# Kernel tuning notes

Hardware: AMD Instinct MI355X
Metric: run time of the kernel (lower is better)

The kernel has to match this reference:

```python
import jax, jax.numpy as jnp
import numpy as np

N = 10000; E = 320000; B = 262144
F_NODE = 64; F_EDGE = 8; H = 4; C = 32
EVO_IN = C * 4 * H + 1      # 513
EVO_HID = 256; EVO_DIM = 64
FLOW_IN = EVO_DIM + 5       # 69
FLOW_HID = 256
SLOPE = 0.01                # torch LeakyReLU default slope
GAT_SLOPE = 0.2             # GATv2 attention LeakyReLU slope
EPS = 1e-5                  # BatchNorm eps


def setup_inputs() -> dict:
    key = jax.random.key(0)
    ks = iter(jax.random.split(key, 64))
    def nrm(shape, scale=1.0):
        return jax.random.normal(next(ks), shape, jnp.float32) * scale
    inp = {}
    inp['x1'] = nrm((N, F_NODE))
    inp['edge_index1'] = jax.random.randint(next(ks), (2, E), 0, N)
    inp['edge_attr1'] = nrm((E, F_EDGE))
    inp['x2'] = nrm((N, F_NODE))
    inp['edge_index2'] = jax.random.randint(next(ks), (2, E), 0, N)
    inp['edge_attr2'] = nrm((E, F_EDGE))
    inp['dist_m'] = jax.random.uniform(next(ks), (N, N), jnp.float32)
    inp['node_visit'] = jax.random.uniform(next(ks), (N, 2), jnp.float32)
    inp['od_nodes'] = jax.random.randint(next(ks), (B, 2), 0, N)
    # GATv2Conv params per snapshot: lin_l, lin_r (bias=True), lin_edge (bias=False), att [H,C], out bias [H*C]
    for p in ('g1', 'g2'):
        s = 1.0 / np.sqrt(F_NODE)
        inp[p + '_Wl'] = nrm((H * C, F_NODE), s)
        inp[p + '_bl'] = jnp.zeros((H * C,), jnp.float32)
        inp[p + '_Wr'] = nrm((H * C, F_NODE), s)
        inp[p + '_br'] = jnp.zeros((H * C,), jnp.float32)
        inp[p + '_We'] = nrm((H * C, F_EDGE), 1.0 / np.sqrt(F_EDGE))
        inp[p + '_att'] = nrm((H, C), 1.0 / np.sqrt(C))
        inp[p + '_bias'] = jnp.zeros((H * C,), jnp.float32)
    # EvoEmbedding (all Linear bias=False)
    inp['e_W1'] = nrm((EVO_HID, EVO_IN), 1.0 / np.sqrt(EVO_IN))
    inp['e_W2'] = nrm((EVO_HID, EVO_HID), 1.0 / np.sqrt(EVO_HID))
    inp['e_W3'] = nrm((EVO_HID, EVO_HID), 1.0 / np.sqrt(EVO_HID))
    inp['e_W4'] = nrm((EVO_HID // 2, EVO_HID), 1.0 / np.sqrt(EVO_HID))
    inp['e_Wout'] = nrm((EVO_DIM, EVO_HID // 2), 1.0 / np.sqrt(EVO_HID // 2))
    # FlowGenerator (Linear bias=False) + BatchNorm affine params
    inp['f_W1'] = nrm((FLOW_HID, FLOW_IN), 1.0 / np.sqrt(FLOW_IN))
    inp['f_W2'] = nrm((FLOW_HID, FLOW_HID), 1.0 / np.sqrt(FLOW_HID))
    inp['f_W3'] = nrm((FLOW_HID, FLOW_HID), 1.0 / np.sqrt(FLOW_HID))
    inp['f_W4'] = nrm((FLOW_HID // 2, FLOW_HID), 1.0 / np.sqrt(FLOW_HID))
    inp['f_Wout'] = nrm((1, FLOW_HID // 2), 1.0 / np.sqrt(FLOW_HID // 2))
    inp['f_g1'] = jnp.ones((FLOW_HID,), jnp.float32);  inp['f_b1'] = jnp.zeros((FLOW_HID,), jnp.float32)
    inp['f_g2'] = jnp.ones((FLOW_HID,), jnp.float32);  inp['f_b2'] = jnp.zeros((FLOW_HID,), jnp.float32)
    inp['f_g3'] = jnp.ones((FLOW_HID,), jnp.float32);  inp['f_b3'] = jnp.zeros((FLOW_HID,), jnp.float32)
    inp['f_g4'] = jnp.ones((FLOW_HID // 2,), jnp.float32); inp['f_b4'] = jnp.zeros((FLOW_HID // 2,), jnp.float32)
    return inp


def _gatv2(x, ei, ea, Wl, bl, Wr, br, We, att, bias):
    src, dst = ei[0], ei[1]
    # self-loops with fill_value='mean': per-target mean of incoming edge_attr
    deg = jax.ops.segment_sum(jnp.ones_like(dst, jnp.float32), dst, N)
    mean_attr = jax.ops.segment_sum(ea, dst, N) / jnp.maximum(deg, 1.0)[:, None]
    loops = jnp.arange(N)
    s = jnp.concatenate([src, loops]); d = jnp.concatenate([dst, loops])
    eaf = jnp.concatenate([ea, mean_attr], axis=0)            # [E+N, F_EDGE]
    xl = (x @ Wl.T + bl).reshape(N, H, C)                     # source transform
    xr = (x @ Wr.T + br).reshape(N, H, C)                     # target transform
    em = (eaf @ We.T).reshape(-1, H, C)
    msg = jax.nn.leaky_relu(xl[s] + xr[d] + em, GAT_SLOPE)    # [E+N, H, C]
    scr = jnp.einsum('ehc,hc->eh', msg, att)                  # [E+N, H]
    mx = jax.ops.segment_max(scr, d, N)
    ex = jnp.exp(scr - mx[d])
    den = jax.ops.segment_sum(ex, d, N)
    alpha = ex / den[d]                                       # softmax over incoming edges
    out = jax.ops.segment_sum(alpha[:, :, None] * xl[s], d, N).reshape(N, H * C) + bias
    return jax.nn.relu(out), alpha


def _evo(v, W1, W2, W3, W4, Wout):
    h = jax.nn.leaky_relu(v @ W1.T, SLOPE)
    h = jax.nn.leaky_relu(h @ W2.T, SLOPE)
    h = jax.nn.leaky_relu(h @ W3.T, SLOPE)
    h = jax.nn.leaky_relu(h @ W4.T, SLOPE)
    return h @ Wout.T


def _bn(x, g, b):
    mu = x.mean(0)
    var = x.var(0)
    return (x - mu) * jax.lax.rsqrt(var + EPS) * g + b


def _flow(v, W1, W2, W3, W4, Wout, g1, b1, g2, b2, g3, b3, g4, b4):
    h = jax.nn.leaky_relu(_bn(v @ W1.T, g1, b1), SLOPE)
    h = jax.nn.leaky_relu(_bn(h @ W2.T, g2, b2), SLOPE)
    h = jax.nn.leaky_relu(_bn(h @ W3.T, g3, b3), SLOPE)
    h = jax.nn.leaky_relu(_bn(h @ W4.T, g4, b4), SLOPE)
    return (h @ Wout.T).squeeze(-1)


def reference(x1, edge_index1, edge_attr1, x2, edge_index2, edge_attr2, dist_m, node_visit, od_nodes,
              g1_Wl, g1_bl, g1_Wr, g1_br, g1_We, g1_att, g1_bias,
              g2_Wl, g2_bl, g2_Wr, g2_br, g2_We, g2_att, g2_bias,
              e_W1, e_W2, e_W3, e_W4, e_Wout,
              f_W1, f_W2, f_W3, f_W4, f_Wout,
              f_g1, f_b1, f_g2, f_b2, f_g3, f_b3, f_g4, f_b4):
    n1, a1 = _gatv2(x1, edge_index1, edge_attr1, g1_Wl, g1_bl, g1_Wr, g1_br, g1_We, g1_att, g1_bias)
    n2, a2 = _gatv2(x2, edge_index2, edge_attr2, g2_Wl, g2_bl, g2_Wr, g2_br, g2_We, g2_att, g2_bias)
    o = od_nodes[:, 0]; dn = od_nodes[:, 1]
    dist = dist_m[o, dn][:, None]                              # fused gather replacing python loop
    feat = jnp.concatenate([n1[o], n1[dn], n2[o], n2[dn], dist], axis=1)  # [B, 513]
    evo = _evo(feat, e_W1, e_W2, e_W3, e_W4, e_Wout)           # [B, EVO_DIM]
    # NOTE: original uses node_visit[:,0] for BOTH o_visit and d_visit (kept faithful)
    ov = node_visit[o, 0:1]; dv = node_visit[dn, 0:1]
    ovn = node_visit[o, 1:2]; dvn = node_visit[dn, 1:2]
    cat = jnp.concatenate([evo, ov, dv, ovn, dvn, dist], axis=1)  # [B, 69]
    inferred = _flow(cat, f_W1, f_W2, f_W3, f_W4, f_Wout, f_g1, f_b1, f_g2, f_b2, f_g3, f_b3, f_g4, f_b4)
    return (inferred, a1, a2, evo)
```

## Files before the change

kernel.cpp:

```cpp
#include <hip/hip_runtime.h>

typedef unsigned short u16;
typedef unsigned int u32;

#define NN 10000
#define NE 320000
#define ET 330000
#define NB 262144

typedef __attribute__((ext_vector_type(8))) short bf16x8;
typedef __attribute__((ext_vector_type(4))) float f32x4;

__device__ __forceinline__ u16 f2b(float f) {
  u32 u = __float_as_uint(f);
  u += 0x7fffu + ((u >> 16) & 1u);
  return (u16)(u >> 16);
}
__device__ __forceinline__ float b2f(u16 h) {
  return __uint_as_float(((u32)h) << 16);
}
__device__ __forceinline__ float lrelu(float v, float s) { return v > 0.f ? v : v * s; }

__device__ __forceinline__ void g2lds16(const void* g, void* l) {
  __builtin_amdgcn_global_load_lds((const __attribute__((address_space(1))) void*)g,
                                   (__attribute__((address_space(3))) void*)l, 16, 0, 0);
}

template <int N> __device__ __forceinline__ void waitv() {
  if constexpr (N == 0) asm volatile("s_waitcnt vmcnt(0)" ::: "memory");
  else if constexpr (N == 1) asm volatile("s_waitcnt vmcnt(1)" ::: "memory");
  else if constexpr (N == 2) asm volatile("s_waitcnt vmcnt(2)" ::: "memory");
  else if constexpr (N == 3) asm volatile("s_waitcnt vmcnt(3)" ::: "memory");
  else if constexpr (N == 4) asm volatile("s_waitcnt vmcnt(4)" ::: "memory");
  else if constexpr (N == 5) asm volatile("s_waitcnt vmcnt(5)" ::: "memory");
  else asm volatile("s_waitcnt vmcnt(6)" ::: "memory");
}
__device__ __forceinline__ void waitl0() { asm volatile("s_waitcnt lgkmcnt(0)" ::: "memory"); }
__device__ __forceinline__ void fence() { asm volatile("" ::: "memory"); }

__global__ __launch_bounds__(256) void k_prep(const float* __restrict__ eW2, const float* __restrict__ eW3,
                                              const float* __restrict__ eW4, const float* __restrict__ eWo,
                                              const float* __restrict__ fW1, const float* __restrict__ fW2,
                                              const float* __restrict__ fW3, const float* __restrict__ fW4,
                                              const float* __restrict__ eW1,
                                              u16* eW2b, u16* eW3b, u16* eW4b, u16* eWob,
                                              u16* fW2b, u16* fW3b, u16* fW4b,
                                              float* W1T, float* w512, u16* combW) {
  const int blk = blockIdx.x, tid = threadIdx.x;
  if (blk < 256) {
    int t = blk * 256 + tid; eW2b[t] = f2b(eW2[t]);
  } else if (blk < 512) {
    int t = (blk - 256) * 256 + tid; eW3b[t] = f2b(eW3[t]);
  } else if (blk < 640) {
    int t = (blk - 512) * 256 + tid; eW4b[t] = f2b(eW4[t]);
  } else if (blk < 672) {
    int t = (blk - 640) * 256 + tid; eWob[t] = f2b(eWo[t]);
  } else if (blk < 928) {
    int t = (blk - 672) * 256 + tid; fW2b[t] = f2b(fW2[t]);
  } else if (blk < 1184) {
    int t = (blk - 928) * 256 + tid; fW3b[t] = f2b(fW3[t]);
  } else if (blk < 1312) {
    int t = (blk - 1184) * 256 + tid; fW4b[t] = f2b(fW4[t]);
  } else if (blk < 1568) {
    int m = blk - 1312;
    for (int k = tid; k < 512; k += 256) W1T[(size_t)k * 256 + m] = eW1[(size_t)m * 513 + k];
  } else if (blk == 1568) {
    w512[tid] = eW1[(size_t)tid * 513 + 512];
  } else {
    int m = blk - 1569;
    int k = tid;
    if (k < 160) {
      float v = 0.f;
      if (k < 128) {
        const float* fr = fW1 + (size_t)m * 69;
        for (int j = 0; j < 64; ++j) v += fr[j] * eWo[(size_t)j * 128 + k];
      } else if (k < 133) {
        v = fW1[(size_t)m * 69 + 64 + (k - 128)];
      }
      combW[(size_t)m * 160 + k] = f2b(v);
    }
  }
}

__global__ __launch_bounds__(256) void k_sprep(const int* __restrict__ od, const float* __restrict__ dm,
                                               const float* __restrict__ nv,
                                               float* __restrict__ distb, u16* __restrict__ bufC) {
  int b = blockIdx.x * 256 + threadIdx.x;
  int o = od[b * 2], d = od[b * 2 + 1];
  float dist = dm[(size_t)o * NN + d];
  distb[b] = dist;
  u16 tmp[32];
  tmp[0] = f2b(nv[o * 2]);
  tmp[1] = f2b(nv[d * 2]);
  tmp[2] = f2b(nv[o * 2 + 1]);
  tmp[3] = f2b(nv[d * 2 + 1]);
  tmp[4] = f2b(dist);
#pragma unroll
  for (int k = 5; k < 32; ++k) tmp[k] = 0;
  u16* p = bufC + (size_t)b * 160 + 128;
#pragma unroll
  for (int k = 0; k < 4; ++k) *(bf16x8*)(p + k * 8) = *(bf16x8*)(tmp + k * 8);
}

__global__ __launch_bounds__(256) void k_count(const int* __restrict__ ei, int* __restrict__ cnt) {
  int t = blockIdx.x * 256 + threadIdx.x;
  if (t >= ET) return;
  int d = (t < NE) ? ei[NE + t] : (t - NE);
  atomicAdd(&cnt[d], 1);
}

__global__ __launch_bounds__(1024) void k_scan(const int* __restrict__ cnt, int* __restrict__ cs) {
  __shared__ int part[1024];
  int tid = threadIdx.x;
  int base = tid * 10;
  int local[10];
  int s = 0;
#pragma unroll
  for (int i = 0; i < 10; ++i) {
    int idx = base + i;
    int v = (idx < NN) ? cnt[idx] : 0;
    local[i] = s; s += v;
  }
  part[tid] = s;
  __syncthreads();
  for (int off = 1; off < 1024; off <<= 1) {
    int v = (tid >= off) ? part[tid - off] : 0;
    __syncthreads();
    part[tid] += v;
    __syncthreads();
  }
  int pre = (tid > 0) ? part[tid - 1] : 0;
#pragma unroll
  for (int i = 0; i < 10; ++i) {
    int idx = base + i;
    if (idx < NN) cs[idx] = pre + local[i];
  }
  if (tid == 1023) cs[NN] = part[1023];
}

__global__ __launch_bounds__(256) void k_fill(const int* __restrict__ ei, const int* __restrict__ cs,
                                              int* __restrict__ wr, int2* __restrict__ csr) {
  int t = blockIdx.x * 256 + threadIdx.x;
  if (t >= ET) return;
  int s, d;
  if (t < NE) { s = ei[t]; d = ei[NE + t]; } else { s = t - NE; d = s; }
  int pos = atomicAdd(&wr[d], 1);
  csr[cs[d] + pos] = make_int2(t, s);
}

__global__ __launch_bounds__(256) void k_asum(const int2* __restrict__ csr, const int* __restrict__ cs,
                                              const float* __restrict__ ea, float* __restrict__ asum) {
  int wid = (blockIdx.x * 256 + threadIdx.x) >> 6;
  int lane = threadIdx.x & 63;
  int beg = cs[wid], end = cs[wid + 1];
  int j = lane & 7, slot = lane >> 3;
  float acc = 0.f;
  for (int i = beg + slot; i < end; i += 8) {
    int e = csr[i].x;
    if (e < NE) acc += ea[(size_t)e * 8 + j];
  }
  acc += __shfl_xor(acc, 8);
  acc += __shfl_xor(acc, 16);
  acc += __shfl_xor(acc, 32);
  if (lane < 8) {
    float dr = (float)(end - beg - 1);
    asum[(size_t)wid * 8 + lane] = acc / fmaxf(dr, 1.f);
  }
}

__global__ __launch_bounds__(256) void k_xlr(const float* __restrict__ x,
                                             const float* __restrict__ Wl, const float* __restrict__ bl,
                                             const float* __restrict__ Wr, const float* __restrict__ br,
                                             float* __restrict__ xl, float* __restrict__ xr) {
  __shared__ float sx[128];
  int nb = blockIdx.x * 2;
  for (int i = threadIdx.x; i < 128; i += 256) sx[i] = x[(size_t)nb * 64 + i];
  __syncthreads();
  int half = threadIdx.x >> 7;
  int node = nb + half;
  int m = threadIdx.x & 127;
  const float* xv = sx + (half << 6);
  float al = bl[m], ar = br[m];
  const float* wl = Wl + (size_t)m * 64;
  const float* wr = Wr + (size_t)m * 64;
#pragma unroll 8
  for (int k = 0; k < 64; ++k) { float xk = xv[k]; al += xk * wl[k]; ar += xk * wr[k]; }
  xl[(size_t)node * 128 + m] = al;
  xr[(size_t)node * 128 + m] = ar;
}

__global__ __launch_bounds__(256) void k_scr(const float* __restrict__ xl, const float* __restrict__ xr,
                                             const int* __restrict__ ei, const float* __restrict__ ea,
                                             const float* __restrict__ mattr,
                                             const float* __restrict__ We, const float* __restrict__ att,
                                             float* __restrict__ scr) {
  const int lane = threadIdx.x & 63;
  const int sub = lane & 31;
  const int half = lane >> 5;
  float4 w0[4], w1[4];
#pragma unroll
  for (int c = 0; c < 4; ++c) {
    const float* wp = We + (size_t)(sub * 4 + c) * 8;
    w0[c] = *(const float4*)wp;
    w1[c] = *(const float4*)(wp + 4);
  }
  const float4 attv = *(const float4*)(att + sub * 4);
  const int gw = (blockIdx.x * 256 + threadIdx.x) >> 6;
  const int nw = gridDim.x * 4;
  for (int p = gw; p < ET / 2; p += nw) {
    int e = p * 2 + half;
    int s, d; const float* ap;
    if (e < NE) { s = ei[e]; d = ei[NE + e]; ap = ea + (size_t)e * 8; }
    else { s = e - NE; d = s; ap = mattr + (size_t)(e - NE) * 8; }
    float4 a0 = *(const float4*)ap;
    float4 a1 = *(const float4*)(ap + 4);
    float4 xlv = *(const float4*)(xl + (size_t)s * 128 + sub * 4);
    float4 xrv = *(const float4*)(xr + (size_t)d * 128 + sub * 4);
    const float* xle = (const float*)&xlv;
    const float* xre = (const float*)&xrv;
    const float* ate = (const float*)&attv;
    float psum = 0.f;
#pragma unroll
    for (int c = 0; c < 4; ++c) {
      float em = a0.x * w0[c].x + a0.y * w0[c].y + a0.z * w0[c].z + a0.w * w0[c].w
               + a1.x * w1[c].x + a1.y * w1[c].y + a1.z * w1[c].z + a1.w * w1[c].w;
      float v = xle[c] + xre[c] + em;
      v = v > 0.f ? v : 0.2f * v;
      psum += v * ate[c];
    }
    psum += __shfl_xor(psum, 1);
    psum += __shfl_xor(psum, 2);
    psum += __shfl_xor(psum, 4);
    if ((sub & 7) == 0) scr[(size_t)e * 4 + (sub >> 3)] = psum;
  }
}

__global__ __launch_bounds__(256) void k_nodered(const float* __restrict__ scr, const int2* __restrict__ csr,
                                                 const int* __restrict__ cs, const float* __restrict__ xl,
                                                 const float* __restrict__ bias,
                                                 float* __restrict__ m_out, float* __restrict__ den_out,
                                                 float* __restrict__ nout) {
  int d = (blockIdx.x * 256 + threadIdx.x) >> 6;
  int lane = threadIdx.x & 63;
  int h0 = lane >> 5;
  int beg = cs[d], end = cs[d + 1];
  float mx0 = -3.4e38f, mx1 = -3.4e38f;
  for (int i = beg; i < end; ++i) {
    int e = csr[i].x;
    mx0 = fmaxf(mx0, scr[(size_t)e * 4 + h0]);
    mx1 = fmaxf(mx1, scr[(size_t)e * 4 + h0 + 2]);
  }
  float acc0 = 0.f, acc1 = 0.f, dn0 = 0.f, dn1 = 0.f;
  for (int i = beg; i < end; ++i) {
    int2 es = csr[i];
    float ex0 = __expf(scr[(size_t)es.x * 4 + h0] - mx0);
    float ex1 = __expf(scr[(size_t)es.x * 4 + h0 + 2] - mx1);
    dn0 += ex0; dn1 += ex1;
    const float* xp = xl + (size_t)es.y * 128;
    acc0 += ex0 * xp[lane];
    acc1 += ex1 * xp[64 + lane];
  }
  if (lane == 0 || lane == 32) {
    m_out[d * 4 + h0] = mx0;     m_out[d * 4 + h0 + 2] = mx1;
    den_out[d * 4 + h0] = dn0;   den_out[d * 4 + h0 + 2] = dn1;
  }
  nout[(size_t)d * 128 + lane] = fmaxf(acc0 / dn0 + bias[lane], 0.f);
  nout[(size_t)d * 128 + 64 + lane] = fmaxf(acc1 / dn1 + bias[64 + lane], 0.f);
}

__global__ __launch_bounds__(256) void k_alpha(const float* __restrict__ scr, const int* __restrict__ ei,
                                               const float* __restrict__ m, const float* __restrict__ den,
                                               float* __restrict__ aout) {
  int t = blockIdx.x * 256 + threadIdx.x;
  if (t >= ET * 4) return;
  int e = t >> 2, h = t & 3;
  int d = (e < NE) ? ei[NE + e] : (e - NE);
  aout[t] = __expf(scr[t] - m[d * 4 + h]) / den[d * 4 + h];
}

__global__ __launch_bounds__(256) void k_qtab(const float* __restrict__ n1, const float* __restrict__ n2,
                                              const float* __restrict__ W1T,
                                              u16* __restrict__ Qo, u16* __restrict__ Qd) {
  __shared__ float s1[2048], s2[2048];
  int nb = blockIdx.x * 16;
  for (int i = threadIdx.x; i < 2048; i += 256) {
    s1[i] = n1[(size_t)nb * 128 + i];
    s2[i] = n2[(size_t)nb * 128 + i];
  }
  __syncthreads();
  int m = threadIdx.x;
  float qo[16], qd[16];
#pragma unroll
  for (int i = 0; i < 16; ++i) { qo[i] = 0.f; qd[i] = 0.f; }
#pragma unroll 2
  for (int k = 0; k < 128; ++k) {
    float w0 = W1T[(size_t)k * 256 + m];
    float w1 = W1T[(size_t)(128 + k) * 256 + m];
    float w2 = W1T[(size_t)(256 + k) * 256 + m];
    float w3 = W1T[(size_t)(384 + k) * 256 + m];
#pragma unroll
    for (int i = 0; i < 16; ++i) {
      float a = s1[i * 128 + k], b = s2[i * 128 + k];
      qo[i] += a * w0 + b * w2;
      qd[i] += a * w1 + b * w3;
    }
  }
#pragma unroll
  for (int i = 0; i < 16; ++i) {
    Qo[(size_t)(nb + i) * 256 + m] = f2b(qo[i]);
    Qd[(size_t)(nb + i) * 256 + m] = f2b(qd[i]);
  }
}

template <int NF, int EPI, int BNA>
__global__ __launch_bounds__(512) void gemm256(const u16* __restrict__ A, const u16* __restrict__ W,
                                               int K, size_t lda,
                                               u16* __restrict__ obf, int ld_bf,
                                               float* __restrict__ stats,
                                               const float* __restrict__ stin, const float* __restrict__ gg,
                                               const float* __restrict__ bb, float invB) {
  constexpr int M = NF * 64;
  constexpr int CPW = 2 + NF / 2;
  __shared__ alignas(16) u16 Alds[2][256 * 32];
  __shared__ alignas(16) u16 Blds[2][M * 32];
  __shared__ float sS[256], sT[256];
  const int tid = threadIdx.x;
  const int lane = tid & 63;
  const int w = tid >> 6;
  const int wr = w >> 2, wc = w & 3;
  const size_t rowBase = (size_t)blockIdx.x * 256;

  if (BNA) {
    for (int c = tid; c < K; c += 512) {
      float mu = stin[c] * invB;
      float var = stin[K + c] * invB - mu * mu;
      float sc = rsqrtf(var + 1e-5f) * gg[c];
      sS[c] = sc;
      sT[c] = bb[c] - mu * sc;
    }
    __syncthreads();
  }

  f32x4 acc[8][NF];
  const f32x4 z4 = {0.f, 0.f, 0.f, 0.f};
#pragma unroll
  for (int m = 0; m < 8; ++m)
#pragma unroll
    for (int n = 0; n < NF; ++n) acc[m][n] = z4;

  const int crow = lane >> 2;
  const int ccol = (lane & 3) << 3;
  const int KT = K >> 5;

  auto stage = [&](int buf, int kb) {
#pragma unroll
    for (int i = 0; i < CPW; ++i) {
      const int c = w * CPW + i;
      if (c < 16) {
        const u16* src = A + (rowBase + (c << 4) + crow) * lda + kb + ccol;
        g2lds16(src, &Alds[buf][(c << 4) << 5]);
// ... 137 lines not shown
  };
  auto writeA = [&](int buf, int kb, bf16x8 r0, bf16x8 r1, bf16x8 r2, bf16x8 r3) {
    float dist = sDist[arow];
    bf16x8 w0, w1;
#pragma unroll
    for (int j = 0; j < 8; ++j) {
      float v = b2f((u16)r0[j]) + b2f((u16)r2[j]) + dist * sW[kb + acol + j];
      w0[j] = (short)f2b(lrelu(v, 0.01f));
      float v2 = b2f((u16)r1[j]) + b2f((u16)r3[j]) + dist * sW[kb + acol + 8 + j];
      w1[j] = (short)f2b(lrelu(v2, 0.01f));
    }
    *(bf16x8*)&Alds[buf][arow * 32 + acol] = w0;
    *(bf16x8*)&Alds[buf][arow * 32 + acol + 8] = w1;
  };

  f32x4 acc[8][4];
  const f32x4 z4 = {0.f, 0.f, 0.f, 0.f};
#pragma unroll
  for (int m = 0; m < 8; ++m)
#pragma unroll
    for (int n = 0; n < 4; ++n) acc[m][n] = z4;

  bf16x8 p0, p1, p2, p3;
  {
    bf16x8 c0, c1, c2, c3;
    loadA(0, c0, c1, c2, c3);
    writeA(0, 0, c0, c1, c2, c3);
  }
  stageB(0, 0);
  fence();
  loadA(32, p0, p1, p2, p3);
  fence();
  waitv<4>();
  waitl0();
  __builtin_amdgcn_s_barrier();

  int cur = 0;
  for (int kt = 0; kt < KT; ++kt) {
    const int kb = kt << 5;
    const bool hasN = kt + 1 < KT, hasNN = kt + 2 < KT;
    bf16x8 bfr[4];
#pragma unroll
    for (int n = 0; n < 4; ++n)
      bfr[n] = *(const bf16x8*)&Blds[cur][((((wc << 2) + n) << 4) + lr) * 32 + lk];
    if (hasN) stageB(cur ^ 1, kb + 32);
    fence();
    bf16x8 q0, q1, q2, q3;
    if (hasNN) loadA(kb + 64, q0, q1, q2, q3);
    fence();
#pragma unroll
    for (int m = 0; m < 8; ++m) {
      bf16x8 af = *(const bf16x8*)&Alds[cur][(((wr << 7) + (m << 4) + lr) << 5) + lk];
#pragma unroll
      for (int n = 0; n < 4; ++n)
        acc[m][n] = __builtin_amdgcn_mfma_f32_16x16x32_bf16(af, bfr[n], acc[m][n], 0, 0, 0);
    }
    if (hasN) {
      if (hasNN) waitv<6>(); else waitv<2>();
      writeA(cur ^ 1, kb + 32, p0, p1, p2, p3);
      p0 = q0; p1 = q1; p2 = q2; p3 = q3;
      if (hasNN) waitv<4>(); else waitv<0>();
      waitl0();
    }
    __builtin_amdgcn_s_barrier();
    cur ^= 1;
  }

#pragma unroll
  for (int m = 0; m < 8; ++m) {
#pragma unroll
    for (int n = 0; n < 4; ++n) {
      const int col = (wc << 6) + (n << 4) + lr;
#pragma unroll
      for (int j = 0; j < 4; ++j) {
        const size_t row = rowBase + (wr << 7) + (m << 4) + (lg << 2) + j;
        float v = acc[m][n][j];
        v = v > 0.f ? v : v * 0.01f;
        obf[row * 256 + col] = f2b(v);
      }
    }
  }
}

template <int NF>
__global__ __launch_bounds__(256) void gemm_f32out(const u16* __restrict__ A, const u16* __restrict__ W,
                                                   int K, size_t lda, int M, float* __restrict__ of32) {
  constexpr int CW = NF * 16;
  __shared__ alignas(16) u16 Alds[2][128 * 32];
  __shared__ alignas(16) u16 Blds[2][CW * 2 * 32];
  const int lane = threadIdx.x & 63;
  const int w = threadIdx.x >> 6;
  const int wr = w >> 1, wc = w & 1;
  const size_t rowBase = (size_t)blockIdx.x * 128;

  f32x4 acc[4][NF];
  const f32x4 z4 = {0.f, 0.f, 0.f, 0.f};
#pragma unroll
  for (int m = 0; m < 4; ++m)
#pragma unroll
    for (int n = 0; n < NF; ++n) acc[m][n] = z4;

  const int sr = (w << 4) + (lane >> 2);
  const int sc = (lane & 3) << 3;
  const int KT = K >> 5;

  auto stage = [&](int buf, int kb) {
#pragma unroll
    for (int i = 0; i < 2; ++i) {
      const u16* src = A + (rowBase + (i << 6) + sr) * lda + kb + sc;
      g2lds16(src, &Alds[buf][((i << 6) + (w << 4)) << 5]);
    }
#pragma unroll
    for (int i = 0; i < NF / 2; ++i) {
      const u16* src = W + (size_t)((i << 6) + sr) * K + kb + sc;
      g2lds16(src, &Blds[buf][((i << 6) + (w << 4)) << 5]);
    }
  };

  stage(0, 0);
  int cur = 0;
  for (int kt = 0; kt < KT; ++kt) {
    if (kt + 1 < KT) {
      stage(cur ^ 1, (kt + 1) << 5);
      asm volatile("s_waitcnt vmcnt(3)" ::: "memory");
    } else {
      asm volatile("s_waitcnt vmcnt(0)" ::: "memory");
    }
    __builtin_amdgcn_s_barrier();
    const int lr = lane & 15, lk = (lane >> 4) << 3;
    bf16x8 af[4], bfr[NF];
#pragma unroll
    for (int m = 0; m < 4; ++m)
      af[m] = *(const bf16x8*)&Alds[cur][(((wr << 6) + (m << 4) + lr) << 5) + lk];
#pragma unroll
    for (int n = 0; n < NF; ++n)
      bfr[n] = *(const bf16x8*)&Blds[cur][((wc * CW + (n << 4) + lr) << 5) + lk];
#pragma unroll
    for (int m = 0; m < 4; ++m)
#pragma unroll
      for (int n = 0; n < NF; ++n)
        acc[m][n] = __builtin_amdgcn_mfma_f32_16x16x32_bf16(af[m], bfr[n], acc[m][n], 0, 0, 0);
    __builtin_amdgcn_s_barrier();
    cur ^= 1;
  }

  const int lr = lane & 15, lg = lane >> 4;
#pragma unroll
  for (int m = 0; m < 4; ++m) {
#pragma unroll
    for (int n = 0; n < NF; ++n) {
      const int col = wc * CW + (n << 4) + lr;
      if (col >= M) continue;
#pragma unroll
      for (int j = 0; j < 4; ++j) {
        const size_t row = rowBase + (wr << 6) + (m << 4) + (lg << 2) + j;
        of32[row * M + col] = acc[m][n][j];
      }
    }
  }
}

__global__ __launch_bounds__(256) void k_fout4(const u16* __restrict__ pre, const float* __restrict__ st,
                                               const float* __restrict__ g, const float* __restrict__ b,
                                               const float* __restrict__ W, float* __restrict__ out,
                                               float invB) {
  __shared__ float smu[128], srs[128], sg[128], sb[128], sw[128];
  if (threadIdx.x < 128) {
    int c = threadIdx.x;
    float mu = st[c] * invB;
    float var = st[128 + c] * invB - mu * mu;
    smu[c] = mu;
    srs[c] = rsqrtf(var + 1e-5f);
    sg[c] = g[c];
    sb[c] = b[c];
    sw[c] = W[c];
  }
  __syncthreads();
  int bi = blockIdx.x * 256 + threadIdx.x;
  const u16* hp = pre + (size_t)bi * 128;
  float acc = 0.f;
#pragma unroll
  for (int k = 0; k < 128; k += 8) {
    bf16x8 u = *(const bf16x8*)(hp + k);
#pragma unroll
    for (int j = 0; j < 8; ++j) {
      int c = k + j;
      float v = (b2f((u16)u[j]) - smu[c]) * srs[c] * sg[c] + sb[c];
      v = b2f(f2b(lrelu(v, 0.01f)));
      acc += v * sw[c];
    }
  }
  out[bi] = acc;
}

extern "C" void kernel_launch(void* const* d_in, const int* in_sizes, int n_in,
                              void* d_out, int out_size, void* d_ws, size_t ws_size,
                              hipStream_t stream) {
  (void)in_sizes; (void)n_in; (void)out_size; (void)ws_size;

  const float* x[2] = {(const float*)d_in[0], (const float*)d_in[3]};
  const int* ei[2] = {(const int*)d_in[1], (const int*)d_in[4]};
  const float* ea[2] = {(const float*)d_in[2], (const float*)d_in[5]};
  const float* dm = (const float*)d_in[6];
  const float* nv = (const float*)d_in[7];
  const int* od = (const int*)d_in[8];
  const float* Wl[2] = {(const float*)d_in[9], (const float*)d_in[16]};
  const float* bl[2] = {(const float*)d_in[10], (const float*)d_in[17]};
  const float* Wr[2] = {(const float*)d_in[11], (const float*)d_in[18]};
  const float* br[2] = {(const float*)d_in[12], (const float*)d_in[19]};
  const float* We[2] = {(const float*)d_in[13], (const float*)d_in[20]};
  const float* att[2] = {(const float*)d_in[14], (const float*)d_in[21]};
  const float* bia[2] = {(const float*)d_in[15], (const float*)d_in[22]};
  const float* eW1 = (const float*)d_in[23];
  const float* eW2 = (const float*)d_in[24];
  const float* eW3 = (const float*)d_in[25];
  const float* eW4 = (const float*)d_in[26];
  const float* eWo = (const float*)d_in[27];
  const float* fW1 = (const float*)d_in[28];
  const float* fW2 = (const float*)d_in[29];
  const float* fW3 = (const float*)d_in[30];
  const float* fW4 = (const float*)d_in[31];
  const float* fWo = (const float*)d_in[32];
  const float* fg[4] = {(const float*)d_in[33], (const float*)d_in[35], (const float*)d_in[37], (const float*)d_in[39]};
  const float* fb[4] = {(const float*)d_in[34], (const float*)d_in[36], (const float*)d_in[38], (const float*)d_in[40]};

  float* out_inf = (float*)d_out;
  float* out_a1 = out_inf + NB;
  float* out_a2 = out_a1 + (size_t)ET * 4;
  float* out_evo = out_a2 + (size_t)ET * 4;

  char* base = (char*)d_ws;
  size_t cur = 0;
  auto carve = [&](size_t bytes) -> char* {
    char* p = base + cur;
    cur += (bytes + 255) & ~(size_t)255;
    return p;
  };
  u16* bufA = (u16*)carve((size_t)NB * 256 * 2);
  u16* bufB = (u16*)carve((size_t)NB * 256 * 2);
  u16* bufC = (u16*)carve((size_t)NB * 160 * 2);
  float* n1 = (float*)carve((size_t)NN * 128 * 4);
  float* n2 = (float*)carve((size_t)NN * 128 * 4);
  u16* Qob = (u16*)carve((size_t)NN * 256 * 2);
  u16* Qdb = (u16*)carve((size_t)NN * 256 * 2);
  float* xl = (float*)carve((size_t)NN * 128 * 4);
  float* xr = (float*)carve((size_t)NN * 128 * 4);
  int* cnt = (int*)carve((size_t)(NN + 1) * 4);
  int* wr = (int*)carve((size_t)NN * 4);
  int* cs = (int*)carve((size_t)(NN + 1) * 4);
  int2* csr = (int2*)carve((size_t)ET * 8);
  float* m_out = (float*)carve((size_t)NN * 4 * 4);
  float* den_out = (float*)carve((size_t)NN * 4 * 4);
  float* asum = (float*)carve((size_t)NN * 8 * 4);
  float* scr = (float*)carve((size_t)ET * 4 * 4);
  float* distb = (float*)carve((size_t)NB * 4);
  float* w512 = (float*)carve(1024);
  float* W1T = (float*)carve(512 * 256 * 4);
  float* stats = (float*)carve(1792 * 4);
  float* st[4] = {stats, stats + 512, stats + 1024, stats + 1536};
  u16* eW2b = (u16*)carve(256 * 256 * 2);
  u16* eW3b = (u16*)carve(256 * 256 * 2);
  u16* eW4b = (u16*)carve(128 * 256 * 2);
  u16* eWob = (u16*)carve(64 * 128 * 2);
  u16* fW2b = (u16*)carve(256 * 256 * 2);
  u16* fW3b = (u16*)carve(256 * 256 * 2);
  u16* fW4b = (u16*)carve(128 * 256 * 2);
  u16* combW = (u16*)carve(256 * 160 * 2);

  k_prep<<<1825, 256, 0, stream>>>(eW2, eW3, eW4, eWo, fW1, fW2, fW3, fW4, eW1,
                                   eW2b, eW3b, eW4b, eWob, fW2b, fW3b, fW4b,
                                   W1T, w512, combW);
  hipMemsetAsync(stats, 0, 1792 * 4, stream);
  k_sprep<<<NB / 256, 256, 0, stream>>>(od, dm, nv, distb, bufC);

  float* nout[2] = {n1, n2};
  float* aout[2] = {out_a1, out_a2};
  const int EB = (ET + 255) / 256;
  const size_t cwSpan = (size_t)((char*)wr - (char*)cnt) + (size_t)NN * 4;
  for (int gi = 0; gi < 2; ++gi) {
    hipMemsetAsync(cnt, 0, cwSpan, stream);
    k_count<<<EB, 256, 0, stream>>>(ei[gi], cnt);
    k_scan<<<1, 1024, 0, stream>>>(cnt, cs);
    k_fill<<<EB, 256, 0, stream>>>(ei[gi], cs, wr, csr);
    k_asum<<<NN / 4, 256, 0, stream>>>(csr, cs, ea[gi], asum);
    k_xlr<<<NN / 2, 256, 0, stream>>>(x[gi], Wl[gi], bl[gi], Wr[gi], br[gi], xl, xr);
    k_scr<<<2048, 256, 0, stream>>>(xl, xr, ei[gi], ea[gi], asum, We[gi], att[gi], scr);
    k_nodered<<<NN / 4, 256, 0, stream>>>(scr, csr, cs, xl, bia[gi], m_out, den_out, nout[gi]);
    k_alpha<<<(ET * 4 + 255) / 256, 256, 0, stream>>>(scr, ei[gi], m_out, den_out, aout[gi]);
  }

  k_qtab<<<NN / 16, 256, 0, stream>>>(n1, n2, W1T, Qob, Qdb);

  const float invB = 1.0f / (float)NB;
  const int GB = NB / 256;
  gemm256_evo<<<GB, 512, 0, stream>>>(eW2b, bufA, Qob, Qdb, od, distb, w512);
  gemm256<4, 0, 0><<<GB, 512, 0, stream>>>(bufA, eW3b, 256, 256, bufB, 256, nullptr,
                                           nullptr, nullptr, nullptr, 0.f);
  gemm256<2, 0, 0><<<GB, 512, 0, stream>>>(bufB, eW4b, 256, 256, bufC, 160, nullptr,
                                           nullptr, nullptr, nullptr, 0.f);
  gemm_f32out<2><<<NB / 128, 256, 0, stream>>>(bufC, eWob, 128, 160, 64, out_evo);

  gemm256<4, 1, 0><<<GB, 512, 0, stream>>>(bufC, combW, 160, 160, bufA, 256, st[0],
                                           nullptr, nullptr, nullptr, 0.f);
  gemm256<4, 1, 1><<<GB, 512, 0, stream>>>(bufA, fW2b, 256, 256, bufB, 256, st[1],
                                           st[0], fg[0], fb[0], invB);
  gemm256<4, 1, 1><<<GB, 512, 0, stream>>>(bufB, fW3b, 256, 256, bufA, 256, st[2],
                                           st[1], fg[1], fb[1], invB);
  gemm256<2, 1, 1><<<GB, 512, 0, stream>>>(bufA, fW4b, 256, 256, bufB, 128, st[3],
                                           st[2], fg[2], fb[2], invB);
  k_fout4<<<NB / 256, 256, 0, stream>>>(bufB, st[3], fg[3], fb[3], fWo, out_inf, invB);
}
```

Measured before the change: 1.386 ms.

## Batch both GAT snapshots into single launches and fuse evo-out with flow layer-1 GEMM

Each graph-preprocessing and GATv2 kernel now handles both snapshots in one launch, with a doubled grid and per-graph buffers, instead of a two-iteration host loop. This halves the launch count and gives small kernels more parallelism. The evo output projection and the first flow layer share the same input (bufC), so they are merged into one 320-column GEMM. That GEMM writes fp32 evo output for the first 64 columns and bf16 pre-activations plus BatchNorm stats for the remaining 256. The cost is more workspace memory and a larger per-block accumulator tile, which may lower occupancy.

Measured after the change: 1.316 ms. -5.0%, faster.

```diff
diff --git a/kernel.cpp b/kernel.cpp
--- a/kernel.cpp
+++ b/kernel.cpp
@@ -43,9 +43,9 @@
                                               const float* __restrict__ fW1, const float* __restrict__ fW2,
                                               const float* __restrict__ fW3, const float* __restrict__ fW4,
                                               const float* __restrict__ eW1,
-                                              u16* eW2b, u16* eW3b, u16* eW4b, u16* eWob,
+                                              u16* eW2b, u16* eW3b, u16* eW4b,
                                               u16* fW2b, u16* fW3b, u16* fW4b,
-                                              float* W1T, float* w512, u16* combW) {
+                                              float* W1T, float* w512, u16* wTail) {
   const int blk = blockIdx.x, tid = threadIdx.x;
   if (blk < 256) {
     int t = blk * 256 + tid; eW2b[t] = f2b(eW2[t]);
@@ -53,21 +53,23 @@
     int t = (blk - 256) * 256 + tid; eW3b[t] = f2b(eW3[t]);
   } else if (blk < 640) {
     int t = (blk - 512) * 256 + tid; eW4b[t] = f2b(eW4[t]);
-  } else if (blk < 672) {
-    int t = (blk - 640) * 256 + tid; eWob[t] = f2b(eWo[t]);
-  } else if (blk < 928) {
-    int t = (blk - 672) * 256 + tid; fW2b[t] = f2b(fW2[t]);
-  } else if (blk < 1184) {
-    int t = (blk - 928) * 256 + tid; fW3b[t] = f2b(fW3[t]);
-  } else if (blk < 1312) {
-    int t = (blk - 1184) * 256 + tid; fW4b[t] = f2b(fW4[t]);
-  } else if (blk < 1568) {
-    int m = blk - 1312;
+  } else if (blk < 896) {
+    int t = (blk - 640) * 256 + tid; fW2b[t] = f2b(fW2[t]);
+  } else if (blk < 1152) {
+    int t = (blk - 896) * 256 + tid; fW3b[t] = f2b(fW3[t]);
+  } else if (blk < 1280) {
+    int t = (blk - 1152) * 256 + tid; fW4b[t] = f2b(fW4[t]);
+  } else if (blk < 1536) {
+    int m = blk - 1280;
     for (int k = tid; k < 512; k += 256) W1T[(size_t)k * 256 + m] = eW1[(size_t)m * 513 + k];
-  } else if (blk == 1568) {
+  } else if (blk == 1536) {
     w512[tid] = eW1[(size_t)tid * 513 + 512];
+  } else if (blk < 1577) {
+    int t = (blk - 1537) * 256 + tid;
+    int r = t / 160, k = t - r * 160;
+    wTail[(size_t)r * 160 + k] = (k < 128) ? f2b(eWo[(size_t)r * 128 + k]) : (u16)0;
   } else {
-    int m = blk - 1569;
+    int m = blk - 1577;
     int k = tid;
     if (k < 160) {
       float v = 0.f;
@@ -77,7 +79,7 @@
       } else if (k < 133) {
         v = fW1[(size_t)m * 69 + 64 + (k - 128)];
       }
-      combW[(size_t)m * 160 + k] = f2b(v);
+      wTail[(size_t)(64 + m) * 160 + k] = f2b(v);
     }
   }
 }
@@ -102,14 +104,19 @@
   for (int k = 0; k < 4; ++k) *(bf16x8*)(p + k * 8) = *(bf16x8*)(tmp + k * 8);
 }
 
-__global__ __launch_bounds__(256) void k_count(const int* __restrict__ ei, int* __restrict__ cnt) {
+__global__ __launch_bounds__(256) void k_count2(const int* __restrict__ ei0, const int* __restrict__ ei1,
+                                                int* __restrict__ cnt) {
   int t = blockIdx.x * 256 + threadIdx.x;
-  if (t >= ET) return;
-  int d = (t < NE) ? ei[NE + t] : (t - NE);
-  atomicAdd(&cnt[d], 1);
-}
-
-__global__ __launch_bounds__(1024) void k_scan(const int* __restrict__ cnt, int* __restrict__ cs) {
+  if (t >= 2 * ET) return;
+  int g = t >= ET; int e = t - g * ET;
+  const int* ei = g ? ei1 : ei0;
+  int d = (e < NE) ? ei[NE + e] : (e - NE);
+  atomicAdd(&cnt[g * NN + d], 1);
+}
+
+__global__ __launch_bounds__(1024) void k_scan2(const int* __restrict__ cnt, int* __restrict__ cs) {
+  const int g = blockIdx.x;
+  cnt += g * NN; cs += g * (NN + 1);
   __shared__ int part[1024];
   int tid = threadIdx.x;
   int base = tid * 10;
@@ -138,25 +145,33 @@
   if (tid == 1023) cs[NN] = part[1023];
 }
 
-__global__ __launch_bounds__(256) void k_fill(const int* __restrict__ ei, const int* __restrict__ cs,
-                                              int* __restrict__ wr, int2* __restrict__ csr) {
+__global__ __launch_bounds__(256) void k_fill2(const int* __restrict__ ei0, const int* __restrict__ ei1,
+                                               const int* __restrict__ cs, int* __restrict__ wr,
+                                               int2* __restrict__ csr) {
   int t = blockIdx.x * 256 + threadIdx.x;
-  if (t >= ET) return;
+  if (t >= 2 * ET) return;
+  int g = t >= ET; int e = t - g * ET;
+  const int* ei = g ? ei1 : ei0;
   int s, d;
-  if (t < NE) { s = ei[t]; d = ei[NE + t]; } else { s = t - NE; d = s; }
-  int pos = atomicAdd(&wr[d], 1);
-  csr[cs[d] + pos] = make_int2(t, s);
-}
-
-__global__ __launch_bounds__(256) void k_asum(const int2* __restrict__ csr, const int* __restrict__ cs,
-                                              const float* __restrict__ ea, float* __restrict__ asum) {
+  if (e < NE) { s = ei[e]; d = ei[NE + e]; } else { s = e - NE; d = s; }
+  int pos = atomicAdd(&wr[g * NN + d], 1);
+  csr[(size_t)g * ET + cs[g * (NN + 1) + d] + pos] = make_int2(e, s);
+}
+
+__global__ __launch_bounds__(256) void k_asum2(const int2* __restrict__ csr, const int* __restrict__ cs,
+                                               const float* __restrict__ ea0, const float* __restrict__ ea1,
+                                               float* __restrict__ asum) {
   int wid = (blockIdx.x * 256 + threadIdx.x) >> 6;
   int lane = threadIdx.x & 63;
-  int beg = cs[wid], end = cs[wid + 1];
+  int g = wid >= NN; int n = wid - g * NN;
+  const float* ea = g ? ea1 : ea0;
+  const int* csg = cs + g * (NN + 1);
+  const int2* csrg = csr + (size_t)g * ET;
+  int beg = csg[n], end = csg[n + 1];
   int j = lane & 7, slot = lane >> 3;
   float acc = 0.f;
   for (int i = beg + slot; i < end; i += 8) {
-    int e = csr[i].x;
+    int e = csrg[i].x;
     if (e < NE) acc += ea[(size_t)e * 8 + j];
   }
   acc += __shfl_xor(acc, 8);
@@ -168,12 +183,22 @@
   }
 }
 
-__global__ __launch_bounds__(256) void k_xlr(const float* __restrict__ x,
-                                             const float* __restrict__ Wl, const float* __restrict__ bl,
-                                             const float* __restrict__ Wr, const float* __restrict__ br,
-                                             float* __restrict__ xl, float* __restrict__ xr) {
+__global__ __launch_bounds__(256) void k_xlr2(const float* __restrict__ x0, const float* __restrict__ x1,
+                                              const float* __restrict__ Wl0, const float* __restrict__ bl0,
+                                              const float* __restrict__ Wr0, const float* __restrict__ br0,
+                                              const float* __restrict__ Wl1, const float* __restrict__ bl1,
+                                              const float* __restrict__ Wr1, const float* __restrict__ br1,
+                                              float* __restrict__ xl, float* __restrict__ xr) {
+  const int g = blockIdx.x >= NN / 2;
+  const int lb = blockIdx.x - g * (NN / 2);
+  const float* x = g ? x1 : x0;
+  const float* Wl = g ? Wl1 : Wl0;
+  const float* bl = g ? bl1 : bl0;
+  const float* Wr = g ? Wr1 : Wr0;
+  const float* br = g ? br1 : br0;
+  xl += (size_t)g * NN * 128; xr += (size_t)g * NN * 128;
   __shared__ float sx[128];
-  int nb = blockIdx.x * 2;
+  int nb = lb * 2;
   for (int i = threadIdx.x; i < 128; i += 256) sx[i] = x[(size_t)nb * 64 + i];
   __syncthreads();
   int half = threadIdx.x >> 7;
@@ -189,11 +214,24 @@
   xr[(size_t)node * 128 + m] = ar;
 }
 
-__global__ __launch_bounds__(256) void k_scr(const float* __restrict__ xl, const float* __restrict__ xr,
-                                             const int* __restrict__ ei, const float* __restrict__ ea,
-                                             const float* __restrict__ mattr,
-                                             const float* __restrict__ We, const float* __restrict__ att,
-                                             float* __restrict__ scr) {
+__global__ __launch_bounds__(256) void k_scr2(const float* __restrict__ xl, const float* __restrict__ xr,
+                                              const int* __restrict__ ei0, const int* __restrict__ ei1,
+                                              const float* __restrict__ ea0, const float* __restrict__ ea1,
+                                              const float* __restrict__ asum,
+                                              const float* __restrict__ We0, const float* __restrict__ We1,
+                                              const float* __restrict__ att0, const float* __restrict__ att1,
+                                              float* __restrict__ scr) {
+  const int g = blockIdx.x >= 2048;
+  const int lb = blockIdx.x - g * 2048;
+  const int* ei = g ? ei1 : ei0;
+  const float* ea = g ? ea1 : ea0;
+  const float* We = g ? We1 : We0;
+  const float* att = g ? att1 : att0;
+  const float* mattr = asum + (size_t)g * NN * 8;
+  const float* xlg = xl + (size_t)g * NN * 128;
+  const float* xrg = xr + (size_t)g * NN * 128;
+  float* scrg = scr + (size_t)g * ET * 4;
+
   const int lane = threadIdx.x & 63;
   const int sub = lane & 31;
   const int half = lane >> 5;
@@ -205,8 +243,8 @@
     w1[c] = *(const float4*)(wp + 4);
   }
   const float4 attv = *(const float4*)(att + sub * 4);
-  const int gw = (blockIdx.x * 256 + threadIdx.x) >> 6;
-  const int nw = gridDim.x * 4;
+  const int gw = (lb * 256 + threadIdx.x) >> 6;
+  const int nw = 2048 * 4;
   for (int p = gw; p < ET / 2; p += nw) {
     int e = p * 2 + half;
     int s, d; const float* ap;
@@ -214,8 +252,8 @@
     else { s = e - NE; d = s; ap = mattr + (size_t)(e - NE) * 8; }
     float4 a0 = *(const float4*)ap;
     float4 a1 = *(const float4*)(ap + 4);
-    float4 xlv = *(const float4*)(xl + (size_t)s * 128 + sub * 4);
-    float4 xrv = *(const float4*)(xr + (size_t)d * 128 + sub * 4);
+    float4 xlv = *(const float4*)(xlg + (size_t)s * 128 + sub * 4);
+    float4 xrv = *(const float4*)(xrg + (size_t)d * 128 + sub * 4);
     const float* xle = (const float*)&xlv;
     const float* xre = (const float*)&xrv;
     const float* ate = (const float*)&attv;
@@ -231,51 +269,67 @@
     psum += __shfl_xor(psum, 1);
     psum += __shfl_xor(psum, 2);
     psum += __shfl_xor(psum, 4);
-    if ((sub & 7) == 0) scr[(size_t)e * 4 + (sub >> 3)] = psum;
-  }
-}
-
-__global__ __launch_bounds__(256) void k_nodered(const float* __restrict__ scr, const int2* __restrict__ csr,
-                                                 const int* __restrict__ cs, const float* __restrict__ xl,
-                                                 const float* __restrict__ bias,
-                                                 float* __restrict__ m_out, float* __restrict__ den_out,
-                                                 float* __restrict__ nout) {
-  int d = (blockIdx.x * 256 + threadIdx.x) >> 6;
+    if ((sub & 7) == 0) scrg[(size_t)e * 4 + (sub >> 3)] = psum;
+  }
+}
+
+__global__ __launch_bounds__(256) void k_nodered2(const float* __restrict__ scr, const int2* __restrict__ csr,
+                                                  const int* __restrict__ cs, const float* __restrict__ xl,
+                                                  const float* __restrict__ bias0, const float* __restrict__ bias1,
+                                                  float* __restrict__ m_out, float* __restrict__ den_out,
+                                                  float* __restrict__ n1, float* __restrict__ n2) {
+  int dd = (blockIdx.x * 256 + threadIdx.x) >> 6;
   int lane = threadIdx.x & 63;
+  int g = dd >= NN; int d = dd - g * NN;
+  const float* scrg = scr + (size_t)g * ET * 4;
+  const int2* csrg = csr + (size_t)g * ET;
+  const int* csg = cs + g * (NN + 1);
+  const float* xlg = xl + (size_t)g * NN * 128;
+  const float* bias = g ? bias1 : bias0;
+  float* mo = m_out + (size_t)g * NN * 4;
+  float* dn = den_out + (size_t)g * NN * 4;
+  float* nout = g ? n2 : n1;
+
   int h0 = lane >> 5;
-  int beg = cs[d], end = cs[d + 1];
+  int beg = csg[d], end = csg[d + 1];
   float mx0 = -3.4e38f, mx1 = -3.4e38f;
   for (int i = beg; i < end; ++i) {
-    int e = csr[i].x;
-    mx0 = fmaxf(mx0, scr[(size_t)e * 4 + h0]);
-    mx1 = fmaxf(mx1, scr[(size_t)e * 4 + h0 + 2]);
+    int e = csrg[i].x;
+    mx0 = fmaxf(mx0, scrg[(size_t)e * 4 + h0]);
+    mx1 = fmaxf(mx1, scrg[(size_t)e * 4 + h0 + 2]);
   }
   float acc0 = 0.f, acc1 = 0.f, dn0 = 0.f, dn1 = 0.f;
   for (int i = beg; i < end; ++i) {
-    int2 es = csr[i];
-    float ex0 = __expf(scr[(size_t)es.x * 4 + h0] - mx0);
-    float ex1 = __expf(scr[(size_t)es.x * 4 + h0 + 2] - mx1);
+    int2 es = csrg[i];
+    float ex0 = __expf(scrg[(size_t)es.x * 4 + h0] - mx0);
+    float ex1 = __expf(scrg[(size_t)es.x * 4 + h0 + 2] - mx1);
     dn0 += ex0; dn1 += ex1;
-    const float* xp = xl + (size_t)es.y * 128;
+    const float* xp = xlg + (size_t)es.y * 128;
     acc0 += ex0 * xp[lane];
     acc1 += ex1 * xp[64 + lane];
   }
   if (lane == 0 || lane == 32) {
-    m_out[d * 4 + h0] = mx0;     m_out[d * 4 + h0 + 2] = mx1;
-    den_out[d * 4 + h0] = dn0;   den_out[d * 4 + h0 + 2] = dn1;
+    mo[d * 4 + h0] = mx0;     mo[d * 4 + h0 + 2] = mx1;
+    dn[d * 4 + h0] = dn0;     dn[d * 4 + h0 + 2] = dn1;
   }
   nout[(size_t)d * 128 + lane] = fmaxf(acc0 / dn0 + bias[lane], 0.f);
   nout[(size_t)d * 128 + 64 + lane] = fmaxf(acc1 / dn1 + bias[64 + lane], 0.f);
 }
 
-__global__ __launch_bounds__(256) void k_alpha(const float* __restrict__ scr, const int* __restrict__ ei,
-                                               const float* __restrict__ m, const float* __restrict__ den,
-                                               float* __restrict__ aout) {
+__global__ __launch_bounds__(256) void k_alpha2(const float* __restrict__ scr,
+                                                const int* __restrict__ ei0, const int* __restrict__ ei1,
+                                                const float* __restrict__ m, const float* __restrict__ den,
+                                                float* __restrict__ a1, float* __restrict__ a2) {
   int t = blockIdx.x * 256 + threadIdx.x;
-  if (t >= ET * 4) return;
-  int e = t >> 2, h = t & 3;
+  if (t >= 2 * ET * 4) return;
+  int g = t >= ET * 4; int tt = t - g * ET * 4;
+  int e = tt >> 2, h = tt & 3;
+  const int* ei = g ? ei1 : ei0;
   int d = (e < NE) ? ei[NE + e] : (e - NE);
-  aout[t] = __expf(scr[t] - m[d * 4 + h]) / den[d * 4 + h];
+  const float* mg = m + (size_t)g * NN * 4;
+  const float* dg = den + (size_t)g * NN * 4;
+  float* aout = g ? a2 : a1;
+  aout[tt] = __expf(scr[(size_t)g * ET * 4 + tt] - mg[d * 4 + h]) / dg[d * 4 + h];
 }
 
 __global__ __launch_bounds__(256) void k_qtab(const float* __restrict__ n1, const float* __restrict__ n2,
@@ -579,38 +633,48 @@
   }
 }
 
-template <int NF>
-__global__ __launch_bounds__(256) void gemm_f32out(const u16* __restrict__ A, const u16* __restrict__ W,
-                                                   int K, size_t lda, int M, float* __restrict__ of32) {
-  constexpr int CW = NF * 16;
-  __shared__ alignas(16) u16 Alds[2][128 * 32];
-  __shared__ alignas(16) u16 Blds[2][CW * 2 * 32];
-  const int lane = threadIdx.x & 63;
-  const int w = threadIdx.x >> 6;
-  const int wr = w >> 1, wc = w & 1;
-  const size_t rowBase = (size_t)blockIdx.x * 128;
-
-  f32x4 acc[4][NF];
+__global__ __launch_bounds__(512) void gemm320(const u16* __restrict__ A, const u16* __restrict__ W,
+                                               float* __restrict__ oevo, u16* __restrict__ opre,
+                                               float* __restrict__ stats) {
+  constexpr int KT = 5;
+  __shared__ alignas(16) u16 Alds[2][256 * 32];
+  __shared__ alignas(16) u16 Blds[2][320 * 32];
+  const int tid = threadIdx.x;
+  const int lane = tid & 63;
+  const int w = tid >> 6;
+  const int wr = w >> 2, wc = w & 3;
+  const size_t rowBase = (size_t)blockIdx.x * 256;
+  const int crow = lane >> 2, ccol = (lane & 3) << 3;
+  const int lr = lane & 15, lk = (lane >> 4) << 3, lg = lane >> 4;
+
+  f32x4 acc[8][5];
   const f32x4 z4 = {0.f, 0.f, 0.f, 0.f};
 #pragma unroll
-  for (int m = 0; m < 4; ++m)
-#pragma unroll
-    for (int n = 0; n < NF; ++n) acc[m][n] = z4;
-
-  const int sr = (w << 4) + (lane >> 2);
-  const int sc = (lane & 3) << 3;
-  const int KT = K >> 5;
+  for (int m = 0; m < 8; ++m)
+#pragma unroll
+    for (int n = 0; n < 5; ++n) acc[m][n] = z4;
 
   auto stage = [&](int buf, int kb) {
 #pragma unroll
     for (int i = 0; i < 2; ++i) {
-      const u16* src = A + (rowBase + (i << 6) + sr) * lda + kb + sc;
-      g2lds16(src, &Alds[buf][((i << 6) + (w << 4)) << 5]);
-    }
-#pragma unroll
-    for (int i = 0; i < NF / 2; ++i) {
-      const u16* src = W + (size_t)((i << 6) + sr) * K + kb + sc;
-      g2lds16(src, &Blds[buf][((i << 6) + (w << 4)) << 5]);
+      int c = w * 2 + i;
+      const u16* src = A + (rowBase + (c << 4) + crow) * 160 + kb + ccol;
+      g2lds16(src, &Alds[buf][(c << 4) << 5]);
+    }
+    if (w < 4) {
+#pragma unroll
+      for (int i = 0; i < 3; ++i) {
+        int c = w * 3 + i;
+        const u16* src = W + (size_t)((c << 4) + crow) * 160 + kb + ccol;
+        g2lds16(src, &Blds[buf][(c << 4) << 5]);
+      }
+    } else {
+#pragma unroll
+      for (int i = 0; i < 2; ++i) {
+        int c = 12 + (w - 4) * 2 + i;
+        const u16* src = W + (size_t)((c << 4) + crow) * 160 + kb + ccol;
+        g2lds16(src, &Blds[buf][(c << 4) << 5]);
+      }
     }
   };
 
@@ -619,39 +683,57 @@
   for (int kt = 0; kt < KT; ++kt) {
     if (kt + 1 < KT) {
       stage(cur ^ 1, (kt + 1) << 5);
-      asm volatile("s_waitcnt vmcnt(3)" ::: "memory");
+      waitv<4>();
     } else {
-      asm volatile("s_waitcnt vmcnt(0)" ::: "memory");
+      waitv<0>();
     }
     __builtin_amdgcn_s_barrier();
-    const int lr = lane & 15, lk = (lane >> 4) << 3;
-    bf16x8 af[4], bfr[NF];
-#pragma unroll
-    for (int m = 0; m < 4; ++m)
-      af[m] = *(const bf16x8*)&Alds[cur][(((wr << 6) + (m << 4) + lr) << 5) + lk];
-#pragma unroll
-    for (int n = 0; n < NF; ++n)
-      bfr[n] = *(const bf16x8*)&Blds[cur][((wc * CW + (n << 4) + lr) << 5) + lk];
-#pragma unroll
-    for (int m = 0; m < 4; ++m)
-#pragma unroll
-      for (int n = 0; n < NF; ++n)
-        acc[m][n] = __builtin_amdgcn_mfma_f32_16x16x32_bf16(af[m], bfr[n], acc[m][n], 0, 0, 0);
+    bf16x8 bfr[5];
+#pragma unroll
+    for (int n = 0; n < 5; ++n)
+      bfr[n] = *(const bf16x8*)&Blds[cur][(((wc * 80 + (n << 4) + lr)) << 5) + lk];
+#pragma unroll
+    for (int m = 0; m < 8; ++m) {
+      bf16x8 af = *(const bf16x8*)&Alds[cur][(((wr << 7) + (m << 4) + lr) << 5) + lk];
+#pragma unroll
+      for (int n = 0; n < 5; ++n)
+        acc[m][n] = __builtin_amdgcn_mfma_f32_16x16x32_bf16(af, bfr[n], acc[m][n], 0, 0, 0);
+    }
     __builtin_amdgcn_s_barrier();
     cur ^= 1;
   }
 
-  const int lr = lane & 15, lg = lane >> 4;
-#pragma unroll
-  for (int m = 0; m < 4; ++m) {
-#pragma unroll
-    for (int n = 0; n < NF; ++n) {
-      const int col = wc * CW + (n << 4) + lr;
-      if (col >= M) continue;
+  float csm[5], cq[5];
+#pragma unroll
+  for (int n = 0; n < 5; ++n) { csm[n] = 0.f; cq[n] = 0.f; }
+#pragma unroll
+  for (int m = 0; m < 8; ++m) {
+#pragma unroll
+    for (int n = 0; n < 5; ++n) {
+      const int col = wc * 80 + (n << 4) + lr;
 #pragma unroll
       for (int j = 0; j < 4; ++j) {
-        const size_t row = rowBase + (wr << 6) + (m << 4) + (lg << 2) + j;
-        of32[row * M + col] = acc[m][n][j];
+        const size_t row = rowBase + (wr << 7) + (m << 4) + (lg << 2) + j;
+        float v = acc[m][n][j];
+        if (col < 64) {
+          oevo[row * 64 + col] = v;
+        } else {
+          opre[row * 256 + (col - 64)] = f2b(v);
+          csm[n] += v; cq[n] += v * v;
+        }
+      }
+    }
+  }
+#pragma unroll
+  for (int n = 0; n < 5; ++n) {
+    float s = csm[n], q = cq[n];
+    s += __shfl_xor(s, 16); s += __shfl_xor(s, 32);
+    q += __shfl_xor(q, 16); q += __shfl_xor(q, 32);
+    if (lane < 16) {
+      const int col = wc * 80 + (n << 4) + lane;
+      if (col >= 64) {
+        atomicAdd(&stats[col - 64], s);
+        atomicAdd(&stats[256 + col - 64], q);
       }
     }
   }
@@ -695,19 +777,29 @@
                               hipStream_t stream) {
   (void)in_sizes; (void)n_in; (void)out_size; (void)ws_size;
 
-  const float* x[2] = {(const float*)d_in[0], (const float*)d_in[3]};
-  const int* ei[2] = {(const int*)d_in[1], (const int*)d_in[4]};
-  const float* ea[2] = {(const float*)d_in[2], (const float*)d_in[5]};
+  const float* x0 = (const float*)d_in[0];
+  const int* ei0 = (const int*)d_in[1];
+  const float* ea0 = (const float*)d_in[2];
+  const float* x1 = (const float*)d_in[3];
+  const int* ei1 = (const int*)d_in[4];
+  const float* ea1 = (const float*)d_in[5];
   const float* dm = (const float*)d_in[6];
   const float* nv = (const float*)d_in[7];
   const int* od = (const int*)d_in[8];
-  const float* Wl[2] = {(const float*)d_in[9], (const float*)d_in[16]};
-  const float* bl[2] = {(const float*)d_in[10], (const float*)d_in[17]};
-  const float* Wr[2] = {(const float*)d_in[11], (const float*)d_in[18]};
-  const float* br[2] = {(const float*)d_in[12], (const float*)d_in[19]};
-  const float* We[2] = {(const float*)d_in[13], (const float*)d_in[20]};
-  const float* att[2] = {(const float*)d_in[14], (const float*)d_in[21]};
-  const float* bia[2] = {(const float*)d_in[15], (const float*)d_in[22]};
+  const float* Wl0 = (const float*)d_in[9];
+  const float* bl0 = (const float*)d_in[10];
+  const float* Wr0 = (const float*)d_in[11];
+  const float* br0 = (const float*)d_in[12];
+  const float* We0 = (const float*)d_in[13];
+  const float* att0 = (const float*)d_in[14];
+  const float* bia0 = (const float*)d_in[15];
+  const float* Wl1 = (const float*)d_in[16];
+  const float* bl1 = (const float*)d_in[17];
+  const float* Wr1 = (const float*)d_in[18];
+  const float* br1 = (const float*)d_in[19];
+  const float* We1 = (const float*)d_in[20];
+  const float* att1 = (const float*)d_in[21];
+  const float* bia1 = (const float*)d_in[22];
   const float* eW1 = (const float*)d_in[23];
   const float* eW2 = (const float*)d_in[24];
   const float* eW3 = (const float*)d_in[25];
@@ -740,16 +832,17 @@
   float* n2 = (float*)carve((size_t)NN * 128 * 4);
   u16* Qob = (u16*)carve((size_t)NN * 256 * 2);
   u16* Qdb = (u16*)carve((size_t)NN * 256 * 2);
-  float* xl = (float*)carve((size_t)NN * 128 * 4);
-  float* xr = (float*)carve((size_t)NN * 128 * 4);
-  int* cnt = (int*)carve((size_t)(NN + 1) * 4);
-  int* wr = (int*)carve((size_t)NN * 4);
-  int* cs = (int*)carve((size_t)(NN + 1) * 4);
-  int2* csr = (int2*)carve((size_t)ET * 8);
-  float* m_out = (float*)carve((size_t)NN * 4 * 4);
-  float* den_out = (float*)carve((size_t)NN * 4 * 4);
-  float* asum = (float*)carve((size_t)NN * 8 * 4);
-  float* scr = (float*)carve((size_t)ET * 4 * 4);
+  float* xl = (float*)carve((size_t)2 * NN * 128 * 4);
+  float* xr = (float*)carve((size_t)2 * NN * 128 * 4);
+  int* cw = (int*)carve((size_t)4 * NN * 4);
+  int* cnt = cw;
+  int* wr = cw + 2 * NN;
+  int* cs = (int*)carve((size_t)2 * (NN + 1) * 4);
+  int2* csr = (int2*)carve((size_t)2 * ET * 8);
+  float* m_out = (float*)carve((size_t)2 * NN * 4 * 4);
+  float* den_out = (float*)carve((size_t)2 * NN * 4 * 4);
+  float* asum = (float*)carve((size_t)2 * NN * 8 * 4);
+  float* scr = (float*)carve((size_t)2 * ET * 4 * 4);
   float* distb = (float*)carve((size_t)NB * 4);
   float* w512 = (float*)carve(1024);
   float* W1T = (float*)carve(512 * 256 * 4);
@@ -758,33 +851,26 @@
   u16* eW2b = (u16*)carve(256 * 256 * 2);
   u16* eW3b = (u16*)carve(256 * 256 * 2);
   u16* eW4b = (u16*)carve(128 * 256 * 2);
-  u16* eWob = (u16*)carve(64 * 128 * 2);
   u16* fW2b = (u16*)carve(256 * 256 * 2);
   u16* fW3b = (u16*)carve(256 * 256 * 2);
   u16* fW4b = (u16*)carve(128 * 256 * 2);
-  u16* combW = (u16*)carve(256 * 160 * 2);
-
-  k_prep<<<1825, 256, 0, stream>>>(eW2, eW3, eW4, eWo, fW1, fW2, fW3, fW4, eW1,
-                                   eW2b, eW3b, eW4b, eWob, fW2b, fW3b, fW4b,
-                                   W1T, w512, combW);
+  u16* wTail = (u16*)carve(320 * 160 * 2);
+
+  k_prep<<<1833, 256, 0, stream>>>(eW2, eW3, eW4, eWo, fW1, fW2, fW3, fW4, eW1,
+                                   eW2b, eW3b, eW4b, fW2b, fW3b, fW4b,
+                                   W1T, w512, wTail);
   hipMemsetAsync(stats, 0, 1792 * 4, stream);
   k_sprep<<<NB / 256, 256, 0, stream>>>(od, dm, nv, distb, bufC);
 
-  float* nout[2] = {n1, n2};
-  float* aout[2] = {out_a1, out_a2};
-  const int EB = (ET + 255) / 256;
-  const size_t cwSpan = (size_t)((char*)wr - (char*)cnt) + (size_t)NN * 4;
-  for (int gi = 0; gi < 2; ++gi) {
-    hipMemsetAsync(cnt, 0, cwSpan, stream);
-    k_count<<<EB, 256, 0, stream>>>(ei[gi], cnt);
-    k_scan<<<1, 1024, 0, stream>>>(cnt, cs);
-    k_fill<<<EB, 256, 0, stream>>>(ei[gi], cs, wr, csr);
-    k_asum<<<NN / 4, 256, 0, stream>>>(csr, cs, ea[gi], asum);
-    k_xlr<<<NN / 2, 256, 0, stream>>>(x[gi], Wl[gi], bl[gi], Wr[gi], br[gi], xl, xr);
-    k_scr<<<2048, 256, 0, stream>>>(xl, xr, ei[gi], ea[gi], asum, We[gi], att[gi], scr);
-    k_nodered<<<NN / 4, 256, 0, stream>>>(scr, csr, cs, xl, bia[gi], m_out, den_out, nout[gi]);
-    k_alpha<<<(ET * 4 + 255) / 256, 256, 0, stream>>>(scr, ei[gi], m_out, den_out, aout[gi]);
-  }
+  hipMemsetAsync(cw, 0, (size_t)4 * NN * 4, stream);
+  k_count2<<<(2 * ET + 255) / 256, 256, 0, stream>>>(ei0, ei1, cnt);
+  k_scan2<<<2, 1024, 0, stream>>>(cnt, cs);
+  k_fill2<<<(2 * ET + 255) / 256, 256, 0, stream>>>(ei0, ei1, cs, wr, csr);
+  k_asum2<<<2 * NN / 4, 256, 0, stream>>>(csr, cs, ea0, ea1, asum);
+  k_xlr2<<<NN, 256, 0, stream>>>(x0, x1, Wl0, bl0, Wr0, br0, Wl1, bl1, Wr1, br1, xl, xr);
+  k_scr2<<<4096, 256, 0, stream>>>(xl, xr, ei0, ei1, ea0, ea1, asum, We0, We1, att0, att1, scr);
+  k_nodered2<<<2 * NN / 4, 256, 0, stream>>>(scr, csr, cs, xl, bia0, bia1, m_out, den_out, n1, n2);
+  k_alpha2<<<(2 * ET * 4 + 255) / 256, 256, 0, stream>>>(scr, ei0, ei1, m_out, den_out, out_a1, out_a2);
 
   k_qtab<<<NN / 16, 256, 0, stream>>>(n1, n2, W1T, Qob, Qdb);
 
@@ -795,10 +881,8 @@
                                            nullptr, nullptr, nullptr, 0.f);
   gemm256<2, 0, 0><<<GB, 512, 0, stream>>>(bufB, eW4b, 256, 256, bufC, 160, nullptr,
                                            nullptr, nullptr, nullptr, 0.f);
-  gemm_f32out<2><<<NB / 128, 256, 0, stream>>>(bufC, eWob, 128, 160, 64, out_evo);
-
-  gemm256<4, 1, 0><<<GB, 512, 0, stream>>>(bufC, combW, 160, 160, bufA, 256, st[0],
-                                           nullptr, nullptr, nullptr, 0.f);
+  gemm320<<<GB, 512, 0, stream>>>(bufC, wTail, out_evo, bufA, st[0]);
+
   gemm256<4, 1, 1><<<GB, 512, 0, stream>>>(bufA, fW2b, 256, 256, bufB, 256, st[1],
                                            st[0], fg[0], fb[0], invB);
   gemm256<4, 1, 1><<<GB, 512, 0, stream>>>(bufB, fW3b, 256, 256, bufA, 256, st[2],
```
